# Kernel tuning notes

Measured on AMD Instinct MI355X. Metric: run time of the kernel, lower is better.

Reference implementation:

```python
import jax, jax.numpy as jnp
import numpy as np

N = 50000   # nodes
E = 640000  # edges
H = 128     # input/hidden dim
C = 40      # classes
L = 2       # gnn layers


def _layernorm(h, g, b, eps=1e-5):
    mu = jnp.mean(h, axis=-1, keepdims=True)
    var = jnp.mean((h - mu) ** 2, axis=-1, keepdims=True)
    return (h - mu) * jax.lax.rsqrt(var + eps) * g + b


def setup_inputs() -> dict:
    key = jax.random.key(0)
    ks = jax.random.split(key, 20)
    s = 0.02
    inp = {
        "x": jax.random.normal(ks[0], (N, H), dtype=jnp.float32),
        "edge_index": jax.random.randint(ks[1], (2, E), 0, N, dtype=jnp.int64),
        # input projection MLP (Linear->ReLU->Dropout(eval)->Linear)
        "proj_w1": jax.random.normal(ks[2], (H, H), dtype=jnp.float32) * s,
        "proj_b1": jnp.zeros((H,), jnp.float32),
        "proj_w2": jax.random.normal(ks[3], (H, H), dtype=jnp.float32) * s,
        "proj_b2": jnp.zeros((H,), jnp.float32),
        "in_norm_g": jnp.ones((H,), jnp.float32),
        "in_norm_b": jnp.zeros((H,), jnp.float32),
        # stacked SAGEConv params: lin_l (on mean-aggregated neighbors, with bias),
        # lin_r (root weight, no bias) -- PyG SAGEConv defaults
        "sage_wl": jax.random.normal(ks[4], (L, H, H), dtype=jnp.float32) * s,
        "sage_bl": jnp.zeros((L, H), jnp.float32),
        "sage_wr": jax.random.normal(ks[5], (L, H, H), dtype=jnp.float32) * s,
        "ln_g": jnp.ones((L, H), jnp.float32),
        "ln_b": jnp.zeros((L, H), jnp.float32),
        # classifier MLP
        "cls_w1": jax.random.normal(ks[6], (H, H), dtype=jnp.float32) * s,
        "cls_b1": jnp.zeros((H,), jnp.float32),
        "cls_w2": jax.random.normal(ks[7], (H, C), dtype=jnp.float32) * s,
        "cls_b2": jnp.zeros((C,), jnp.float32),
    }
    return inp


def reference(x, edge_index, proj_w1, proj_b1, proj_w2, proj_b2,
              in_norm_g, in_norm_b, sage_wl, sage_bl, sage_wr,
              ln_g, ln_b, cls_w1, cls_b1, cls_w2, cls_b2):
    src = edge_index[0]  # message sources x_j
    dst = edge_index[1]  # aggregation targets
    # in-degree counts for mean aggregation (isolated nodes -> 0 output)
    cnt = jax.ops.segment_sum(jnp.ones((E,), jnp.float32), dst, num_segments=N)
    inv_cnt = jnp.where(cnt > 0, 1.0 / jnp.maximum(cnt, 1.0), 0.0)[:, None]

    # input projection + norm (dropout is identity in eval mode)
    h = jax.nn.relu(x @ proj_w1 + proj_b1) @ proj_w2 + proj_b2
    h = _layernorm(h, in_norm_g, in_norm_b)

    for l in range(L):
        msg_sum = jax.ops.segment_sum(h[src], dst, num_segments=N)  # [N,H]
        agg = msg_sum * inv_cnt  # mean aggregation
        h_next = agg @ sage_wl[l] + sage_bl[l] + h @ sage_wr[l]  # SAGEConv
        h_next = jax.nn.relu(h_next)
        h = _layernorm(h + h_next, ln_g[l], ln_b[l])  # residual + LayerNorm

    logits = jax.nn.relu(h @ cls_w1 + cls_b1) @ cls_w2 + cls_b2
    return (logits, h)
```

## Files before the change

kernel.cpp:

```cpp
#include <hip/hip_runtime.h>


namespace {

constexpr int NN = 50000;
constexpr int EE = 640000;
constexpr int HH = 128;
constexpr int CC = 40;
constexpr int SCAN_NB = (NN + 255) / 256;
constexpr int MG = (NN + 127) / 128;
constexpr int DEGB = (EE + 255) / 256;

typedef unsigned short u16;
typedef __attribute__((ext_vector_type(8))) short s16x8;
typedef __attribute__((ext_vector_type(8))) unsigned short u16x8;
typedef __attribute__((ext_vector_type(4))) float f32x4;

__device__ __forceinline__ float b2f(u16 h) {
  unsigned int u = ((unsigned int)h) << 16;
  return __builtin_bit_cast(float, u);
}
__device__ __forceinline__ u16 f2b(float f) {
  unsigned int u = __builtin_bit_cast(unsigned int, f);
  u += 0x7FFFu + ((u >> 16) & 1u);
  return (u16)(u >> 16);
}

__device__ __forceinline__ s16x8 ldsw(const u16* base, int n, int k0) {
  return *reinterpret_cast<const s16x8*>(base + n * 128 + (((k0 ^ n) & 15) << 3));
}
__device__ __forceinline__ void stsw(u16* base, int r, int c, u16 v) {
  base[r * 128 + ((((c >> 3) ^ r) & 15) << 3) + (c & 7)] = v;
}
template <int NGRAN>
__device__ __forceinline__ void stage(const u16* __restrict__ src, u16* dst, int tid) {
#pragma unroll
  for (int i = 0; i < (NGRAN + 255) / 256; ++i) {
    const int gi = i * 256 + tid;
    if ((NGRAN & 255) == 0 || gi < NGRAN) {
      const int n = gi >> 4, k0 = gi & 15;
      const u16x8 v = *reinterpret_cast<const u16x8*>(src + gi * 8);
      *reinterpret_cast<u16x8*>(dst + n * 128 + (((k0 ^ n) & 15) << 3)) = v;
    }
  }
}

__global__ void k_pre(const float* __restrict__ pw1, const float* __restrict__ pw2,
                      const float* __restrict__ swl, const float* __restrict__ swr,
                      const float* __restrict__ cw1, const float* __restrict__ cw2,
                      u16* __restrict__ wt, int* __restrict__ cnt) {
  int flat = blockIdx.x * 256 + threadIdx.x;
  const int SEVEN = 7 * 16384;
  const int WDOM = SEVEN + CC * 128;
  if (flat < SEVEN) {
    int id = flat >> 14;
    int off = flat & 16383;
    int n = off >> 7, k = off & 127;
    const float* s;
    switch (id) {
      case 0: s = pw1; break;
      case 1: s = pw2; break;
      case 2: s = swl; break;
      case 3: s = swl + 16384; break;
      case 4: s = swr; break;
      case 5: s = swr + 16384; break;
      default: s = cw1; break;
    }
    wt[(size_t)id * 16384 + n * 128 + k] = f2b(s[k * 128 + n]);
  } else if (flat < WDOM) {
    int off = flat - SEVEN;
    int n = off >> 7, k = off & 127;
    wt[(size_t)7 * 16384 + n * 128 + k] = f2b(cw2[k * CC + n]);
  } else {
    int i = flat - WDOM;
    if (i < NN) cnt[i] = 0;
  }
}

__global__ void k_scan_block(const int* __restrict__ cnt, int* __restrict__ rowptr,
                             int* __restrict__ bsum, float* __restrict__ inv) {
  __shared__ int s[256];
  const int t = threadIdx.x;
  const int i = blockIdx.x * 256 + t;
  const int v = i < NN ? cnt[i] : 0;
  s[t] = v;
  __syncthreads();
  for (int off = 1; off < 256; off <<= 1) {
    int add = t >= off ? s[t - off] : 0;
    __syncthreads();
    s[t] += add;
    __syncthreads();
  }
  if (i < NN) {
    rowptr[i] = s[t] - v;
    inv[i] = v > 0 ? 1.0f / (float)v : 0.0f;
  }
  if (t == 255) bsum[blockIdx.x] = s[255];
}

__global__ void k_scan_add(int* __restrict__ rowptr, const int* __restrict__ bsum) {
  __shared__ int s[256];
  const int t = threadIdx.x;
  const int v = t < SCAN_NB ? bsum[t] : 0;
  s[t] = v;
  __syncthreads();
  for (int off = 1; off < 256; off <<= 1) {
    int add = t >= off ? s[t - off] : 0;
    __syncthreads();
    s[t] += add;
    __syncthreads();
  }
  const int boff = blockIdx.x == 0 ? 0 : s[blockIdx.x - 1];
  const int i = blockIdx.x * 256 + t;
  if (i < NN) rowptr[i] += boff;
  if (i == 0) rowptr[NN] = EE;
}

__global__ void k_fill(const int* __restrict__ ei, const int* __restrict__ rowptr,
                       const int* __restrict__ rank, int* __restrict__ col) {
  int e = blockIdx.x * 256 + threadIdx.x;
  if (e >= EE) return;
  const int d = ei[EE + e];
  col[rowptr[d] + rank[e]] = ei[e];
}

__global__ __launch_bounds__(256) void k_gather_q(
    const u16* __restrict__ hb, const int* __restrict__ rowptr,
    const int* __restrict__ col, const float* __restrict__ inv,
    u16* __restrict__ agg) {
  const int tid = threadIdx.x;
  const int node = blockIdx.x * 16 + (tid >> 4);
  if (node >= NN) return;
  const int ln = tid & 15;
  const int cl = ln * 8;
  const int start = rowptr[node];
  const int end = rowptr[node + 1];
  float a[8] = {0.f, 0.f, 0.f, 0.f, 0.f, 0.f, 0.f, 0.f};
  int i = start;
  for (; i + 8 <= end; i += 8) {
    const int s0 = col[i], s1 = col[i + 1], s2 = col[i + 2], s3 = col[i + 3];
    const int s4 = col[i + 4], s5 = col[i + 5], s6 = col[i + 6], s7 = col[i + 7];
    const u16x8 v0 = *reinterpret_cast<const u16x8*>(&hb[(size_t)s0 * HH + cl]);
    const u16x8 v1 = *reinterpret_cast<const u16x8*>(&hb[(size_t)s1 * HH + cl]);
    const u16x8 v2 = *reinterpret_cast<const u16x8*>(&hb[(size_t)s2 * HH + cl]);
    const u16x8 v3 = *reinterpret_cast<const u16x8*>(&hb[(size_t)s3 * HH + cl]);
    const u16x8 v4 = *reinterpret_cast<const u16x8*>(&hb[(size_t)s4 * HH + cl]);
    const u16x8 v5 = *reinterpret_cast<const u16x8*>(&hb[(size_t)s5 * HH + cl]);
    const u16x8 v6 = *reinterpret_cast<const u16x8*>(&hb[(size_t)s6 * HH + cl]);
    const u16x8 v7 = *reinterpret_cast<const u16x8*>(&hb[(size_t)s7 * HH + cl]);
#pragma unroll
    for (int k = 0; k < 8; ++k)
      a[k] += ((b2f(v0[k]) + b2f(v1[k])) + (b2f(v2[k]) + b2f(v3[k]))) +
              ((b2f(v4[k]) + b2f(v5[k])) + (b2f(v6[k]) + b2f(v7[k])));
  }
  if (i + 4 <= end) {
    const int s0 = col[i], s1 = col[i + 1], s2 = col[i + 2], s3 = col[i + 3];
    const u16x8 v0 = *reinterpret_cast<const u16x8*>(&hb[(size_t)s0 * HH + cl]);
    const u16x8 v1 = *reinterpret_cast<const u16x8*>(&hb[(size_t)s1 * HH + cl]);
    const u16x8 v2 = *reinterpret_cast<const u16x8*>(&hb[(size_t)s2 * HH + cl]);
    const u16x8 v3 = *reinterpret_cast<const u16x8*>(&hb[(size_t)s3 * HH + cl]);
#pragma unroll
    for (int k = 0; k < 8; ++k)
      a[k] += (b2f(v0[k]) + b2f(v1[k])) + (b2f(v2[k]) + b2f(v3[k]));
    i += 4;
  }
  for (; i < end; ++i) {
    const u16x8 v0 = *reinterpret_cast<const u16x8*>(&hb[(size_t)col[i] * HH + cl]);
#pragma unroll
    for (int k = 0; k < 8; ++k) a[k] += b2f(v0[k]);
  }
  const float sc = inv[node];
  u16x8 o;
#pragma unroll
  for (int k = 0; k < 8; ++k) o[k] = f2b(a[k] * sc);
  *reinterpret_cast<u16x8*>(&agg[(size_t)node * HH + cl]) = o;
}

__global__ __launch_bounds__(256) void k_mlp_deg(
    const float* __restrict__ x, const u16* __restrict__ WT1,
    const float* __restrict__ pb1, const u16* __restrict__ WT2,
    const float* __restrict__ pb2, const float* __restrict__ lg,
    const float* __restrict__ lb, u16* __restrict__ hb,
    const int* __restrict__ ei, int* __restrict__ cnt, int* __restrict__ rank) {
  __shared__ u16 lds[32768];
  if (blockIdx.x >= MG) {
    const int e = (blockIdx.x - MG) * 256 + threadIdx.x;
    if (e < EE) rank[e] = atomicAdd(&cnt[ei[EE + e]], 1);
    return;
  }
  u16* wreg = lds;
  u16* t1r = lds + 16384;
  const int tid = threadIdx.x;
  const int wv = tid >> 6, ln = tid & 63;
  const int lrow = ln & 15, kg = ln >> 4;
  const int tbase = blockIdx.x * 128 + wv * 32;
  const int lb0 = wv * 32;
  const int ar0 = min(tbase + lrow, NN - 1);
  const int ar1 = min(tbase + 16 + lrow, NN - 1);

  stage<2048>(WT1, wreg, tid);
  __syncthreads();

  f32x4 acc0[8], acc1[8];
#pragma unroll
  for (int cf = 0; cf < 8; ++cf) {
    acc0[cf] = (f32x4){0.f, 0.f, 0.f, 0.f};
    acc1[cf] = (f32x4){0.f, 0.f, 0.f, 0.f};
  }
#pragma unroll
  for (int ks = 0; ks < 4; ++ks) {
    const float4* p0 = reinterpret_cast<const float4*>(x + (size_t)ar0 * 128 + ks * 32 + kg * 8);
    const float4* p1 = reinterpret_cast<const float4*>(x + (size_t)ar1 * 128 + ks * 32 + kg * 8);
    float4 x0 = p0[0], x1 = p0[1], y0 = p1[0], y1 = p1[1];
    s16x8 a0, a1;
    a0[0] = (short)f2b(x0.x); a0[1] = (short)f2b(x0.y); a0[2] = (short)f2b(x0.z); a0[3] = (short)f2b(x0.w);
    a0[4] = (short)f2b(x1.x); a0[5] = (short)f2b(x1.y); a0[6] = (short)f2b(x1.z); a0[7] = (short)f2b(x1.w);
    a1[0] = (short)f2b(y0.x); a1[1] = (short)f2b(y0.y); a1[2] = (short)f2b(y0.z); a1[3] = (short)f2b(y0.w);
    a1[4] = (short)f2b(y1.x); a1[5] = (short)f2b(y1.y); a1[6] = (short)f2b(y1.z); a1[7] = (short)f2b(y1.w);
#pragma unroll
    for (int cf = 0; cf < 8; ++cf) {
      const s16x8 bf = ldsw(wreg, cf * 16 + lrow, ks * 4 + kg);
      acc0[cf] = __builtin_amdgcn_mfma_f32_16x16x32_bf16(a0, bf, acc0[cf], 0, 0, 0);
      acc1[cf] = __builtin_amdgcn_mfma_f32_16x16x32_bf16(a1, bf, acc1[cf], 0, 0, 0);
    }
  }
  {
    float bb[8];
#pragma unroll
    for (int cf = 0; cf < 8; ++cf) bb[cf] = pb1[cf * 16 + lrow];
#pragma unroll
    for (int t = 0; t < 2; ++t)
#pragma unroll
      for (int j = 0; j < 4; ++j) {
        const int lr = lb0 + t * 16 + kg * 4 + j;
#pragma unroll
        for (int cf = 0; cf < 8; ++cf)
          stsw(t1r, lr, cf * 16 + lrow, f2b(fmaxf((t ? acc1[cf][j] : acc0[cf][j]) + bb[cf], 0.0f)));
      }
  }
  __syncthreads();
  stage<2048>(WT2, wreg, tid);
  __syncthreads();

  f32x4 c0[8], c1[8];
#pragma unroll
  for (int cf = 0; cf < 8; ++cf) {
    c0[cf] = (f32x4){0.f, 0.f, 0.f, 0.f};
    c1[cf] = (f32x4){0.f, 0.f, 0.f, 0.f};
  }
#pragma unroll
  for (int ks = 0; ks < 4; ++ks) {
    const s16x8 a0 = ldsw(t1r, lb0 + lrow, ks * 4 + kg);
    const s16x8 a1 = ldsw(t1r, lb0 + 16 + lrow, ks * 4 + kg);
#pragma unroll
    for (int cf = 0; cf < 8; ++cf) {
      const s16x8 bf = ldsw(wreg, cf * 16 + lrow, ks * 4 + kg);
      c0[cf] = __builtin_amdgcn_mfma_f32_16x16x32_bf16(a0, bf, c0[cf], 0, 0, 0);
      c1[cf] = __builtin_amdgcn_mfma_f32_16x16x32_bf16(a1, bf, c1[cf], 0, 0, 0);
    }
  }

  float bb[8], gm[8], gb[8];
#pragma unroll
  for (int cf = 0; cf < 8; ++cf) {
    const int c = cf * 16 + lrow;
    bb[cf] = pb2[c];
    gm[cf] = lg[c];
    gb[cf] = lb[c];
  }
#pragma unroll
  for (int t = 0; t < 2; ++t)
#pragma unroll
    for (int j = 0; j < 4; ++j) {
      const int r = tbase + t * 16 + kg * 4 + j;
      float v[8];
#pragma unroll
      for (int cf = 0; cf < 8; ++cf) v[cf] = (t ? c1[cf][j] : c0[cf][j]) + bb[cf];
      float s = 0.f;
#pragma unroll
      for (int cf = 0; cf < 8; ++cf) s += v[cf];
      s += __shfl_xor(s, 1); s += __shfl_xor(s, 2);
      s += __shfl_xor(s, 4); s += __shfl_xor(s, 8);
      const float mu = s * (1.0f / 128);
      float q = 0.f;
#pragma unroll
      for (int cf = 0; cf < 8; ++cf) { const float d = v[cf] - mu; q += d * d; }
      q += __shfl_xor(q, 1); q += __shfl_xor(q, 2);
      q += __shfl_xor(q, 4); q += __shfl_xor(q, 8);
      const float istd = rsqrtf(q * (1.0f / 128) + 1e-5f);
      if (r < NN) {
#pragma unroll
        for (int cf = 0; cf < 8; ++cf)
          hb[(size_t)r * 128 + cf * 16 + lrow] = f2b((v[cf] - mu) * istd * gm[cf] + gb[cf]);
      }
    }
}

__global__ __launch_bounds__(256) void k_sage0(
    const u16* __restrict__ agg, const u16* __restrict__ hb,
    const u16* __restrict__ WTl, const u16* __restrict__ WTr,
    const float* __restrict__ bl, const float* __restrict__ lg,
    const float* __restrict__ lb, u16* __restrict__ hb_out) {
  __shared__ u16 lds[32768];
  u16* wl = lds;
  u16* wr = lds + 16384;
  const int tid = threadIdx.x;
  const int wv = tid >> 6, ln = tid & 63;
  const int lrow = ln & 15, kg = ln >> 4;
  const int tbase = blockIdx.x * 128 + wv * 32;
  const int ar0 = min(tbase + lrow, NN - 1);
  const int ar1 = min(tbase + 16 + lrow, NN - 1);

  stage<2048>(WTl, wl, tid);
  stage<2048>(WTr, wr, tid);
  __syncthreads();

  f32x4 acc0[8], acc1[8];
#pragma unroll
  for (int cf = 0; cf < 8; ++cf) {
    acc0[cf] = (f32x4){0.f, 0.f, 0.f, 0.f};
    acc1[cf] = (f32x4){0.f, 0.f, 0.f, 0.f};
  }
#pragma unroll
  for (int ks = 0; ks < 4; ++ks) {
    const s16x8 g0 = *reinterpret_cast<const s16x8*>(agg + (size_t)ar0 * 128 + ks * 32 + kg * 8);
    const s16x8 g1 = *reinterpret_cast<const s16x8*>(agg + (size_t)ar1 * 128 + ks * 32 + kg * 8);
    const s16x8 h0 = *reinterpret_cast<const s16x8*>(hb + (size_t)ar0 * 128 + ks * 32 + kg * 8);
    const s16x8 h1 = *reinterpret_cast<const s16x8*>(hb + (size_t)ar1 * 128 + ks * 32 + kg * 8);
#pragma unroll
    for (int cf = 0; cf < 8; ++cf) {
      const s16x8 bwl = ldsw(wl, cf * 16 + lrow, ks * 4 + kg);
      const s16x8 bwr = ldsw(wr, cf * 16 + lrow, ks * 4 + kg);
      acc0[cf] = __builtin_amdgcn_mfma_f32_16x16x32_bf16(g0, bwl, acc0[cf], 0, 0, 0);
      acc0[cf] = __builtin_amdgcn_mfma_f32_16x16x32_bf16(h0, bwr, acc0[cf], 0, 0, 0);
      acc1[cf] = __builtin_amdgcn_mfma_f32_16x16x32_bf16(g1, bwl, acc1[cf], 0, 0, 0);
      acc1[cf] = __builtin_amdgcn_mfma_f32_16x16x32_bf16(h1, bwr, acc1[cf], 0, 0, 0);
    }
  }

  float bb[8], gm[8], gb[8];
#pragma unroll
  for (int cf = 0; cf < 8; ++cf) {
    const int c = cf * 16 + lrow;
    bb[cf] = bl[c];
    gm[cf] = lg[c];
    gb[cf] = lb[c];
  }
#pragma unroll
  for (int t = 0; t < 2; ++t)
#pragma unroll
    for (int j = 0; j < 4; ++j) {
      const int r = tbase + t * 16 + kg * 4 + j;
      const int rs = r < NN ? r : NN - 1;
      float v[8];
#pragma unroll
      for (int cf = 0; cf < 8; ++cf) {
        const int c = cf * 16 + lrow;
        v[cf] = b2f(hb[(size_t)rs * 128 + c]) +
                fmaxf((t ? acc1[cf][j] : acc0[cf][j]) + bb[cf], 0.0f);
      }
      float s = 0.f;
#pragma unroll
      for (int cf = 0; cf < 8; ++cf) s += v[cf];
      s += __shfl_xor(s, 1); s += __shfl_xor(s, 2);
      s += __shfl_xor(s, 4); s += __shfl_xor(s, 8);
      const float mu = s * (1.0f / 128);
      float q = 0.f;
#pragma unroll
      for (int cf = 0; cf < 8; ++cf) { const float d = v[cf] - mu; q += d * d; }
      q += __shfl_xor(q, 1); q += __shfl_xor(q, 2);
      q += __shfl_xor(q, 4); q += __shfl_xor(q, 8);
      const float istd = rsqrtf(q * (1.0f / 128) + 1e-5f);
      if (r < NN) {
#pragma unroll
        for (int cf = 0; cf < 8; ++cf)
          hb_out[(size_t)r * 128 + cf * 16 + lrow] = f2b((v[cf] - mu) * istd * gm[cf] + gb[cf]);
      }
    }
}

__global__ __launch_bounds__(256) void k_sage_cls(
    const u16* __restrict__ agg, const u16* __restrict__ hb,
    const u16* __restrict__ WTl, const u16* __restrict__ WTr,
    const float* __restrict__ bl, const float* __restrict__ lg,
    const float* __restrict__ lb,
    const u16* __restrict__ Wc1, const float* __restrict__ cb1,
    const u16* __restrict__ Wc2, const float* __restrict__ cb2,
    float* __restrict__ out_h, float* __restrict__ logits) {
  __shared__ u16 lds[37888];
  u16* wl = lds;
  u16* wr = lds + 16384;
  u16* w2 = lds + 32768;
  const int tid = threadIdx.x;
  const int wv = tid >> 6, ln = tid & 63;
  const int lrow = ln & 15, kg = ln >> 4;
  const int tbase = blockIdx.x * 128 + wv * 32;
  const int lb0 = wv * 32;
  const int ar0 = min(tbase + lrow, NN - 1);
  const int ar1 = min(tbase + 16 + lrow, NN - 1);

  stage<2048>(WTl, wl, tid);
  stage<2048>(WTr, wr, tid);
  stage<640>(Wc2, w2, tid);
  __syncthreads();

  f32x4 acc0[8], acc1[8];
#pragma unroll
  for (int cf = 0; cf < 8; ++cf) {
    acc0[cf] = (f32x4){0.f, 0.f, 0.f, 0.f};
    acc1[cf] = (f32x4){0.f, 0.f, 0.f, 0.f};
  }
#pragma unroll
  for (int ks = 0; ks < 4; ++ks) {
    const s16x8 g0 = *reinterpret_cast<const s16x8*>(agg + (size_t)ar0 * 128 + ks * 32 + kg * 8);
    const s16x8 g1 = *reinterpret_cast<const s16x8*>(agg + (size_t)ar1 * 128 + ks * 32 + kg * 8);
    const s16x8 h0 = *reinterpret_cast<const s16x8*>(hb + (size_t)ar0 * 128 + ks * 32 + kg * 8);
    const s16x8 h1 = *reinterpret_cast<const s16x8*>(hb + (size_t)ar1 * 128 + ks * 32 + kg * 8);
#pragma unroll
    for (int cf = 0; cf < 8; ++cf) {
      const s16x8 bwl = ldsw(wl, cf * 16 + lrow, ks * 4 + kg);
      const s16x8 bwr = ldsw(wr, cf * 16 + lrow, ks * 4 + kg);
      acc0[cf] = __builtin_amdgcn_mfma_f32_16x16x32_bf16(g0, bwl, acc0[cf], 0, 0, 0);
      acc0[cf] = __builtin_amdgcn_mfma_f32_16x16x32_bf16(h0, bwr, acc0[cf], 0, 0, 0);
      acc1[cf] = __builtin_amdgcn_mfma_f32_16x16x32_bf16(g1, bwl, acc1[cf], 0, 0, 0);
      acc1[cf] = __builtin_amdgcn_mfma_f32_16x16x32_bf16(h1, bwr, acc1[cf], 0, 0, 0);
    }
  }
  __syncthreads();

  {
    float bb[8], gm[8], gb[8];
#pragma unroll
    for (int cf = 0; cf < 8; ++cf) {
      const int c = cf * 16 + lrow;
      bb[cf] = bl[c];
      gm[cf] = lg[c];
      gb[cf] = lb[c];
    }
#pragma unroll
    for (int t = 0; t < 2; ++t)
#pragma unroll
      for (int j = 0; j < 4; ++j) {
        const int r = tbase + t * 16 + kg * 4 + j;
        const int rs = r < NN ? r : NN - 1;
        const int lr = lb0 + t * 16 + kg * 4 + j;
        float v[8];
#pragma unroll
        for (int cf = 0; cf < 8; ++cf) {
          const int c = cf * 16 + lrow;
          v[cf] = b2f(hb[(size_t)rs * 128 + c]) +
                  fmaxf((t ? acc1[cf][j] : acc0[cf][j]) + bb[cf], 0.0f);
        }
        float s = 0.f;
#pragma unroll
        for (int cf = 0; cf < 8; ++cf) s += v[cf];
        s += __shfl_xor(s, 1); s += __shfl_xor(s, 2);
        s += __shfl_xor(s, 4); s += __shfl_xor(s, 8);
        const float mu = s * (1.0f / 128);
        float q = 0.f;
#pragma unroll
        for (int cf = 0; cf < 8; ++cf) { const float d = v[cf] - mu; q += d * d; }
        q += __shfl_xor(q, 1); q += __shfl_xor(q, 2);
        q += __shfl_xor(q, 4); q += __shfl_xor(q, 8);
        const float istd = rsqrtf(q * (1.0f / 128) + 1e-5f);
#pragma unroll
        for (int cf = 0; cf < 8; ++cf) {
          const int c = cf * 16 + lrow;
          const float o = (v[cf] - mu) * istd * gm[cf] + gb[cf];
          stsw(wl, lr, c, f2b(o));
          if (r < NN) out_h[(size_t)r * 128 + c] = o;
        }
      }
  }
  stage<2048>(Wc1, wr, tid);
  __syncthreads();

  float cb1v[8];
#pragma unroll
  for (int cf = 0; cf < 8; ++cf) cb1v[cf] = cb1[cf * 16 + lrow];

#pragma unroll
  for (int t = 0; t < 2; ++t) {
    const int rb = lb0 + t * 16;
    f32x4 a3[8];
#pragma unroll
    for (int cf = 0; cf < 8; ++cf) a3[cf] = (f32x4){0.f, 0.f, 0.f, 0.f};
#pragma unroll
    for (int ks = 0; ks < 4; ++ks) {
      const s16x8 a = ldsw(wl, rb + lrow, ks * 4 + kg);
#pragma unroll
      for (int cf = 0; cf < 8; ++cf) {
        const s16x8 bf = ldsw(wr, cf * 16 + lrow, ks * 4 + kg);
        a3[cf] = __builtin_amdgcn_mfma_f32_16x16x32_bf16(a, bf, a3[cf], 0, 0, 0);
      }
    }
#pragma unroll
    for (int j = 0; j < 4; ++j)
#pragma unroll
      for (int cf = 0; cf < 8; ++cf)
        stsw(wl, rb + kg * 4 + j, cf * 16 + lrow, f2b(fmaxf(a3[cf][j] + cb1v[cf], 0.0f)));

    f32x4 a2[3];
#pragma unroll
    for (int cf = 0; cf < 3; ++cf) a2[cf] = (f32x4){0.f, 0.f, 0.f, 0.f};
#pragma unroll
    for (int ks = 0; ks < 4; ++ks) {
      const s16x8 a = ldsw(wl, rb + lrow, ks * 4 + kg);
#pragma unroll
      for (int cf = 0; cf < 3; ++cf) {
        const int bn = min(cf * 16 + lrow, CC - 1);
        const s16x8 bf = ldsw(w2, bn, ks * 4 + kg);
        a2[cf] = __builtin_amdgcn_mfma_f32_16x16x32_bf16(a, bf, a2[cf], 0, 0, 0);
      }
    }
#pragma unroll
    for (int j = 0; j < 4; ++j) {
      const int r = tbase + t * 16 + kg * 4 + j;
      if (r < NN) {
#pragma unroll
        for (int cf = 0; cf < 3; ++cf) {
          const int c = cf * 16 + lrow;
          if (c < CC) logits[(size_t)r * CC + c] = a2[cf][j] + cb2[c];
        }
      }
    }
  }
}

}

extern "C" void kernel_launch(void* const* d_in, const int* in_sizes, int n_in,
                              void* d_out, int out_size, void* d_ws, size_t ws_size,
                              hipStream_t stream) {
  (void)in_sizes; (void)n_in; (void)out_size; (void)ws_size;
  const float* x   = (const float*)d_in[0];
  const int*   ei  = (const int*)d_in[1];
  const float* pw1 = (const float*)d_in[2];
  const float* pb1 = (const float*)d_in[3];
  const float* pw2 = (const float*)d_in[4];
  const float* pb2 = (const float*)d_in[5];
  const float* ing = (const float*)d_in[6];
  const float* inb = (const float*)d_in[7];
  const float* swl = (const float*)d_in[8];
  const float* sbl = (const float*)d_in[9];
  const float* swr = (const float*)d_in[10];
  const float* lng = (const float*)d_in[11];
  const float* lnb = (const float*)d_in[12];
  const float* cw1 = (const float*)d_in[13];
  const float* cb1 = (const float*)d_in[14];
  const float* cw2 = (const float*)d_in[15];
  const float* cb2 = (const float*)d_in[16];

  float* out_logits = (float*)d_out;
  float* out_h = out_logits + (size_t)NN * CC;

  const size_t NNH = (size_t)NN * HH;
  u16*   hb   = (u16*)d_ws;
  u16*   bufA = hb + NNH;
  u16*   wt   = bufA + NNH;
  int*   cnt    = (int*)(wt + 8 * 16384);
  float* inv    = (float*)(cnt + NN);
  int*   rowptr = (int*)(inv + NN);
  int*   bsum   = rowptr + NN + 1;
  int*   colarr = bsum + 256;
  int*   rankar = colarr + EE;

  const int PRE_B = (7 * 16384 + CC * 128 + NN + 255) / 256;
  k_pre<<<PRE_B, 256, 0, stream>>>(pw1, pw2, swl, swr, cw1, cw2, wt, cnt);

  k_mlp_deg<<<MG + DEGB, 256, 0, stream>>>(
      x, wt + 0 * 16384, pb1, wt + 1 * 16384, pb2, ing, inb, hb, ei, cnt, rankar);

  k_scan_block<<<SCAN_NB, 256, 0, stream>>>(cnt, rowptr, bsum, inv);
  k_scan_add<<<SCAN_NB, 256, 0, stream>>>(rowptr, bsum);
  k_fill<<<(EE + 255) / 256, 256, 0, stream>>>(ei, rowptr, rankar, colarr);

  k_gather_q<<<(NN + 15) / 16, 256, 0, stream>>>(hb, rowptr, colarr, inv, bufA);
  k_sage0<<<(NN + 127) / 128, 256, 0, stream>>>(
      bufA, hb, wt + 2 * 16384, wt + 4 * 16384, sbl, lng, lnb, hb);

  k_gather_q<<<(NN + 15) / 16, 256, 0, stream>>>(hb, rowptr, colarr, inv, bufA);
  k_sage_cls<<<(NN + 127) / 128, 256, 0, stream>>>(
      bufA, hb, wt + 3 * 16384, wt + 5 * 16384, sbl + HH, lng + HH, lnb + HH,
      wt + 6 * 16384, cb1, wt + 7 * 16384, cb2, out_h, out_logits);
}
```

Baseline: 153.6 us.

## Gather neighbor features from an FP8 copy and fold weight prep into MLP launch

The epilogues of the input MLP and the first SAGE layer now also write an FP8 copy of h, with each lane's eight columns packed in a strided (column-interleaved) order. The gather kernel reads that copy, halving the bytes fetched per random neighbor row, and writes the bf16 aggregate back in standard column order. Conversion of the SAGE and classifier weights moves from the pre-kernel into extra blocks of the MLP/degree launch, shrinking the first kernel. The trade is lower precision in the aggregated messages (FP8 instead of bf16) plus an extra write of the FP8 buffer in the producing kernels.

```diff
diff --git a/kernel.cpp b/kernel.cpp
--- a/kernel.cpp
+++ b/kernel.cpp
@@ -10,11 +10,13 @@
 constexpr int SCAN_NB = (NN + 255) / 256;
 constexpr int MG = (NN + 127) / 128;
 constexpr int DEGB = (EE + 255) / 256;
+constexpr int WPB = (5 * 16384 + CC * 128 + 255) / 256;
 
 typedef unsigned short u16;
 typedef __attribute__((ext_vector_type(8))) short s16x8;
 typedef __attribute__((ext_vector_type(8))) unsigned short u16x8;
 typedef __attribute__((ext_vector_type(4))) float f32x4;
+typedef __attribute__((ext_vector_type(2))) float f32x2;
 
 __device__ __forceinline__ float b2f(u16 h) {
   unsigned int u = ((unsigned int)h) << 16;
@@ -24,6 +26,23 @@
   unsigned int u = __builtin_bit_cast(unsigned int, f);
   u += 0x7FFFu + ((u >> 16) & 1u);
   return (u16)(u >> 16);
+}
+
+__device__ __forceinline__ uint2 pack_fp8(const float* v) {
+  int w0 = 0, w1 = 0;
+  w0 = __builtin_amdgcn_cvt_pk_fp8_f32(v[0], v[1], w0, false);
+  w0 = __builtin_amdgcn_cvt_pk_fp8_f32(v[2], v[3], w0, true);
+  w1 = __builtin_amdgcn_cvt_pk_fp8_f32(v[4], v[5], w1, false);
+  w1 = __builtin_amdgcn_cvt_pk_fp8_f32(v[6], v[7], w1, true);
+  return make_uint2((unsigned)w0, (unsigned)w1);
+}
+__device__ __forceinline__ void acc_fp8(float* a, uint2 p) {
+  const f32x2 f0 = __builtin_amdgcn_cvt_pk_f32_fp8((int)p.x, false);
+  const f32x2 f1 = __builtin_amdgcn_cvt_pk_f32_fp8((int)p.x, true);
+  const f32x2 f2 = __builtin_amdgcn_cvt_pk_f32_fp8((int)p.y, false);
+  const f32x2 f3 = __builtin_amdgcn_cvt_pk_f32_fp8((int)p.y, true);
+  a[0] += f0.x; a[1] += f0.y; a[2] += f1.x; a[3] += f1.y;
+  a[4] += f2.x; a[5] += f2.y; a[6] += f3.x; a[7] += f3.y;
 }
 
 __device__ __forceinline__ s16x8 ldsw(const u16* base, int n, int k0) {
@@ -46,33 +65,17 @@
 }
 
 __global__ void k_pre(const float* __restrict__ pw1, const float* __restrict__ pw2,
-                      const float* __restrict__ swl, const float* __restrict__ swr,
-                      const float* __restrict__ cw1, const float* __restrict__ cw2,
                       u16* __restrict__ wt, int* __restrict__ cnt) {
   int flat = blockIdx.x * 256 + threadIdx.x;
-  const int SEVEN = 7 * 16384;
-  const int WDOM = SEVEN + CC * 128;
-  if (flat < SEVEN) {
+  const int TWO = 2 * 16384;
+  if (flat < TWO) {
     int id = flat >> 14;
     int off = flat & 16383;
     int n = off >> 7, k = off & 127;
-    const float* s;
-    switch (id) {
-      case 0: s = pw1; break;
-      case 1: s = pw2; break;
-      case 2: s = swl; break;
-      case 3: s = swl + 16384; break;
-      case 4: s = swr; break;
-      case 5: s = swr + 16384; break;
-      default: s = cw1; break;
-    }
+    const float* s = id == 0 ? pw1 : pw2;
     wt[(size_t)id * 16384 + n * 128 + k] = f2b(s[k * 128 + n]);
-  } else if (flat < WDOM) {
-    int off = flat - SEVEN;
-    int n = off >> 7, k = off & 127;
-    wt[(size_t)7 * 16384 + n * 128 + k] = f2b(cw2[k * CC + n]);
   } else {
-    int i = flat - WDOM;
+    int i = flat - TWO;
     if (i < NN) cnt[i] = 0;
   }
 }
@@ -124,8 +127,8 @@
   col[rowptr[d] + rank[e]] = ei[e];
 }
 
-__global__ __launch_bounds__(256) void k_gather_q(
-    const u16* __restrict__ hb, const int* __restrict__ rowptr,
+__global__ __launch_bounds__(256) void k_gather8(
+    const unsigned char* __restrict__ h8, const int* __restrict__ rowptr,
     const int* __restrict__ col, const float* __restrict__ inv,
     u16* __restrict__ agg) {
   const int tid = threadIdx.x;
@@ -138,42 +141,33 @@
   float a[8] = {0.f, 0.f, 0.f, 0.f, 0.f, 0.f, 0.f, 0.f};
   int i = start;
   for (; i + 8 <= end; i += 8) {
-    const int s0 = col[i], s1 = col[i + 1], s2 = col[i + 2], s3 = col[i + 3];
-    const int s4 = col[i + 4], s5 = col[i + 5], s6 = col[i + 6], s7 = col[i + 7];
-    const u16x8 v0 = *reinterpret_cast<const u16x8*>(&hb[(size_t)s0 * HH + cl]);
-    const u16x8 v1 = *reinterpret_cast<const u16x8*>(&hb[(size_t)s1 * HH + cl]);
-    const u16x8 v2 = *reinterpret_cast<const u16x8*>(&hb[(size_t)s2 * HH + cl]);
-    const u16x8 v3 = *reinterpret_cast<const u16x8*>(&hb[(size_t)s3 * HH + cl]);
-    const u16x8 v4 = *reinterpret_cast<const u16x8*>(&hb[(size_t)s4 * HH + cl]);
-    const u16x8 v5 = *reinterpret_cast<const u16x8*>(&hb[(size_t)s5 * HH + cl]);
-    const u16x8 v6 = *reinterpret_cast<const u16x8*>(&hb[(size_t)s6 * HH + cl]);
-    const u16x8 v7 = *reinterpret_cast<const u16x8*>(&hb[(size_t)s7 * HH + cl]);
-#pragma unroll
-    for (int k = 0; k < 8; ++k)
-      a[k] += ((b2f(v0[k]) + b2f(v1[k])) + (b2f(v2[k]) + b2f(v3[k]))) +
-              ((b2f(v4[k]) + b2f(v5[k])) + (b2f(v6[k]) + b2f(v7[k])));
+    const uint2 p0 = *reinterpret_cast<const uint2*>(&h8[(size_t)col[i] * 128 + cl]);
+    const uint2 p1 = *reinterpret_cast<const uint2*>(&h8[(size_t)col[i + 1] * 128 + cl]);
+    const uint2 p2 = *reinterpret_cast<const uint2*>(&h8[(size_t)col[i + 2] * 128 + cl]);
+    const uint2 p3 = *reinterpret_cast<const uint2*>(&h8[(size_t)col[i + 3] * 128 + cl]);
+    const uint2 p4 = *reinterpret_cast<const uint2*>(&h8[(size_t)col[i + 4] * 128 + cl]);
+    const uint2 p5 = *reinterpret_cast<const uint2*>(&h8[(size_t)col[i + 5] * 128 + cl]);
+    const uint2 p6 = *reinterpret_cast<const uint2*>(&h8[(size_t)col[i + 6] * 128 + cl]);
+    const uint2 p7 = *reinterpret_cast<const uint2*>(&h8[(size_t)col[i + 7] * 128 + cl]);
+    acc_fp8(a, p0); acc_fp8(a, p1); acc_fp8(a, p2); acc_fp8(a, p3);
+    acc_fp8(a, p4); acc_fp8(a, p5); acc_fp8(a, p6); acc_fp8(a, p7);
   }
   if (i + 4 <= end) {
-    const int s0 = col[i], s1 = col[i + 1], s2 = col[i + 2], s3 = col[i + 3];
-    const u16x8 v0 = *reinterpret_cast<const u16x8*>(&hb[(size_t)s0 * HH + cl]);
-    const u16x8 v1 = *reinterpret_cast<const u16x8*>(&hb[(size_t)s1 * HH + cl]);
-    const u16x8 v2 = *reinterpret_cast<const u16x8*>(&hb[(size_t)s2 * HH + cl]);
-    const u16x8 v3 = *reinterpret_cast<const u16x8*>(&hb[(size_t)s3 * HH + cl]);
-#pragma unroll
-    for (int k = 0; k < 8; ++k)
-      a[k] += (b2f(v0[k]) + b2f(v1[k])) + (b2f(v2[k]) + b2f(v3[k]));
+    const uint2 p0 = *reinterpret_cast<const uint2*>(&h8[(size_t)col[i] * 128 + cl]);
+    const uint2 p1 = *reinterpret_cast<const uint2*>(&h8[(size_t)col[i + 1] * 128 + cl]);
+    const uint2 p2 = *reinterpret_cast<const uint2*>(&h8[(size_t)col[i + 2] * 128 + cl]);
+    const uint2 p3 = *reinterpret_cast<const uint2*>(&h8[(size_t)col[i + 3] * 128 + cl]);
+    acc_fp8(a, p0); acc_fp8(a, p1); acc_fp8(a, p2); acc_fp8(a, p3);
     i += 4;
   }
   for (; i < end; ++i) {
-    const u16x8 v0 = *reinterpret_cast<const u16x8*>(&hb[(size_t)col[i] * HH + cl]);
-#pragma unroll
-    for (int k = 0; k < 8; ++k) a[k] += b2f(v0[k]);
+    const uint2 p0 = *reinterpret_cast<const uint2*>(&h8[(size_t)col[i] * 128 + cl]);
+    acc_fp8(a, p0);
   }
   const float sc = inv[node];
-  u16x8 o;
-#pragma unroll
-  for (int k = 0; k < 8; ++k) o[k] = f2b(a[k] * sc);
-  *reinterpret_cast<u16x8*>(&agg[(size_t)node * HH + cl]) = o;
+#pragma unroll
+  for (int k = 0; k < 8; ++k)
+    agg[(size_t)node * 128 + k * 16 + ln] = f2b(a[k] * sc);
 }
 
 __global__ __launch_bounds__(256) void k_mlp_deg(
@@ -181,11 +175,41 @@
     const float* __restrict__ pb1, const u16* __restrict__ WT2,
     const float* __restrict__ pb2, const float* __restrict__ lg,
     const float* __restrict__ lb, u16* __restrict__ hb,
-    const int* __restrict__ ei, int* __restrict__ cnt, int* __restrict__ rank) {
+    unsigned char* __restrict__ h8,
+    const int* __restrict__ ei, int* __restrict__ cnt, int* __restrict__ rank,
+    const float* __restrict__ swl, const float* __restrict__ swr,
+    const float* __restrict__ cw1, const float* __restrict__ cw2,
+    u16* __restrict__ wt) {
   __shared__ u16 lds[32768];
   if (blockIdx.x >= MG) {
-    const int e = (blockIdx.x - MG) * 256 + threadIdx.x;
-    if (e < EE) rank[e] = atomicAdd(&cnt[ei[EE + e]], 1);
+    const int rb = blockIdx.x - MG;
+    if (rb < DEGB) {
+      const int e = rb * 256 + threadIdx.x;
+      if (e < EE) rank[e] = atomicAdd(&cnt[ei[EE + e]], 1);
+    } else {
+      const int flat = (rb - DEGB) * 256 + threadIdx.x;
+      const int FIVE = 5 * 16384;
+      if (flat < FIVE) {
+        int id = flat >> 14;
+        int off = flat & 16383;
+        int n = off >> 7, k = off & 127;
+        const float* s;
+        switch (id) {
+          case 0: s = swl; break;
+          case 1: s = swl + 16384; break;
+          case 2: s = swr; break;
+          case 3: s = swr + 16384; break;
+          default: s = cw1; break;
+        }
+        wt[(size_t)(id + 2) * 16384 + n * 128 + k] = f2b(s[k * 128 + n]);
+      } else {
+        int off = flat - FIVE;
+        if (off < CC * 128) {
+          int n = off >> 7, k = off & 127;
+          wt[(size_t)7 * 16384 + n * 128 + k] = f2b(cw2[k * CC + n]);
+        }
+      }
+    }
     return;
   }
   u16* wreg = lds;
@@ -289,9 +313,13 @@
       q += __shfl_xor(q, 4); q += __shfl_xor(q, 8);
       const float istd = rsqrtf(q * (1.0f / 128) + 1e-5f);
       if (r < NN) {
-#pragma unroll
-        for (int cf = 0; cf < 8; ++cf)
-          hb[(size_t)r * 128 + cf * 16 + lrow] = f2b((v[cf] - mu) * istd * gm[cf] + gb[cf]);
+        float ov[8];
+#pragma unroll
+        for (int cf = 0; cf < 8; ++cf) {
+          ov[cf] = (v[cf] - mu) * istd * gm[cf] + gb[cf];
+          hb[(size_t)r * 128 + cf * 16 + lrow] = f2b(ov[cf]);
+        }
+        *reinterpret_cast<uint2*>(&h8[(size_t)r * 128 + lrow * 8]) = pack_fp8(ov);
       }
     }
 }
@@ -300,7 +328,8 @@
     const u16* __restrict__ agg, const u16* __restrict__ hb,
     const u16* __restrict__ WTl, const u16* __restrict__ WTr,
     const float* __restrict__ bl, const float* __restrict__ lg,
-    const float* __restrict__ lb, u16* __restrict__ hb_out) {
+    const float* __restrict__ lb, u16* __restrict__ hb_out,
+    unsigned char* __restrict__ h8) {
   __shared__ u16 lds[32768];
   u16* wl = lds;
   u16* wr = lds + 16384;
@@ -372,9 +401,13 @@
       q += __shfl_xor(q, 4); q += __shfl_xor(q, 8);
       const float istd = rsqrtf(q * (1.0f / 128) + 1e-5f);
       if (r < NN) {
-#pragma unroll
-        for (int cf = 0; cf < 8; ++cf)
-          hb_out[(size_t)r * 128 + cf * 16 + lrow] = f2b((v[cf] - mu) * istd * gm[cf] + gb[cf]);
+        float ov[8];
+#pragma unroll
+        for (int cf = 0; cf < 8; ++cf) {
+          ov[cf] = (v[cf] - mu) * istd * gm[cf] + gb[cf];
+          hb_out[(size_t)r * 128 + cf * 16 + lrow] = f2b(ov[cf]);
+        }
+        *reinterpret_cast<uint2*>(&h8[(size_t)r * 128 + lrow * 8]) = pack_fp8(ov);
       }
     }
 }
@@ -564,22 +597,24 @@
   int*   bsum   = rowptr + NN + 1;
   int*   colarr = bsum + 256;
   int*   rankar = colarr + EE;
-
-  const int PRE_B = (7 * 16384 + CC * 128 + NN + 255) / 256;
-  k_pre<<<PRE_B, 256, 0, stream>>>(pw1, pw2, swl, swr, cw1, cw2, wt, cnt);
-
-  k_mlp_deg<<<MG + DEGB, 256, 0, stream>>>(
-      x, wt + 0 * 16384, pb1, wt + 1 * 16384, pb2, ing, inb, hb, ei, cnt, rankar);
+  unsigned char* h8 = (unsigned char*)(rankar + EE);
+
+  const int PRE_B = (2 * 16384 + NN + 255) / 256;
+  k_pre<<<PRE_B, 256, 0, stream>>>(pw1, pw2, wt, cnt);
+
+  k_mlp_deg<<<MG + DEGB + WPB, 256, 0, stream>>>(
+      x, wt + 0 * 16384, pb1, wt + 1 * 16384, pb2, ing, inb, hb, h8,
+      ei, cnt, rankar, swl, swr, cw1, cw2, wt);
 
   k_scan_block<<<SCAN_NB, 256, 0, stream>>>(cnt, rowptr, bsum, inv);
   k_scan_add<<<SCAN_NB, 256, 0, stream>>>(rowptr, bsum);
   k_fill<<<(EE + 255) / 256, 256, 0, stream>>>(ei, rowptr, rankar, colarr);
 
-  k_gather_q<<<(NN + 15) / 16, 256, 0, stream>>>(hb, rowptr, colarr, inv, bufA);
+  k_gather8<<<(NN + 15) / 16, 256, 0, stream>>>(h8, rowptr, colarr, inv, bufA);
   k_sage0<<<(NN + 127) / 128, 256, 0, stream>>>(
-      bufA, hb, wt + 2 * 16384, wt + 4 * 16384, sbl, lng, lnb, hb);
-
-  k_gather_q<<<(NN + 15) / 16, 256, 0, stream>>>(hb, rowptr, colarr, inv, bufA);
+      bufA, hb, wt + 2 * 16384, wt + 4 * 16384, sbl, lng, lnb, hb, h8);
+
+  k_gather8<<<(NN + 15) / 16, 256, 0, stream>>>(h8, rowptr, colarr, inv, bufA);
   k_sage_cls<<<(NN + 127) / 128, 256, 0, stream>>>(
       bufA, hb, wt + 3 * 16384, wt + 5 * 16384, sbl + HH, lng + HH, lnb + HH,
       wt + 6 * 16384, cb1, wt + 7 * 16384, cb2, out_h, out_logits);
```

Result: faster. 142.9 us (median of 2 runs) (-7.0%).
